# Performance work log

Hardware: AMD Instinct MI355X
Metric: run time of the kernel (lower is better)

The kernel has to match this reference:

```python
import jax, jax.numpy as jnp
import numpy as np

GROUPS = 32
EPS = 1e-5


def setup_inputs() -> dict:
    key = jax.random.key(0)
    ks = jax.random.split(key, 7)
    B, C, H, W = 32, 512, 32, 32
    x = jax.random.normal(ks[0], (B, C, H, W), dtype=jnp.float32)
    # GroupNorm affine params
    gn_w = jnp.ones((C,), dtype=jnp.float32)
    gn_b = jnp.zeros((C,), dtype=jnp.float32)
    # 1x1 Conv1d == matmul over channel dim
    qkv_w = jax.random.normal(ks[1], (3 * C, C), dtype=jnp.float32) * (C ** -0.5)
    qkv_b = jax.random.normal(ks[2], (3 * C,), dtype=jnp.float32) * 0.02
    proj_w = jax.random.normal(ks[3], (C, C), dtype=jnp.float32) * (C ** -0.5)
    proj_b = jax.random.normal(ks[4], (C,), dtype=jnp.float32) * 0.02
    return {"x": x, "gn_w": gn_w, "gn_b": gn_b, "qkv_w": qkv_w,
            "qkv_b": qkv_b, "proj_w": proj_w, "proj_b": proj_b}


def _group_norm(x, w, b):
    B, C, H, W = x.shape
    xg = x.reshape(B, GROUPS, C // GROUPS, H, W)
    mean = xg.mean(axis=(2, 3, 4), keepdims=True)
    var = xg.var(axis=(2, 3, 4), keepdims=True)
    xg = (xg - mean) * jax.lax.rsqrt(var + EPS)
    return xg.reshape(B, C, H, W) * w[None, :, None, None] + b[None, :, None, None]


def reference(x, gn_w, gn_b, qkv_w, qkv_b, proj_w, proj_b):
    B, C, H, W = x.shape
    h = _group_norm(x, gn_w, gn_b).reshape(B, C, H * W)  # [B, C, N]
    qkv = jnp.einsum('oc,bcn->bon', qkv_w, h) + qkv_b[None, :, None]  # [B, 3C, N]
    q, k, v = jnp.split(qkv, 3, axis=1)
    scale = C ** (-0.5)
    # scores: q^T k  -> [B, N, N]
    attn = jax.nn.softmax(jnp.einsum('bcn,bcm->bnm', q, k) * scale, axis=-1)
    # h = v @ attn^T -> [B, C, N]
    h = jnp.einsum('bcm,bnm->bcn', v, attn)
    h = jnp.einsum('oc,bcn->bon', proj_w, h) + proj_b[None, :, None]
    return x + h.reshape(B, C, H, W)
```

## Files before the change

### kernel.cpp

```cpp
#include <hip/hip_runtime.h>
#include <stdint.h>

typedef __bf16 bf16;
typedef __bf16 bf16x4 __attribute__((ext_vector_type(4)));
typedef __bf16 bf16x8 __attribute__((ext_vector_type(8)));
typedef float f32x4 __attribute__((ext_vector_type(4)));

#define CN 524288
#define NPIX 1024
#define CCH 512

__device__ __forceinline__ void gload_lds16(const void* g, void* l) {
  auto gp = reinterpret_cast<const __attribute__((address_space(1))) uint32_t*>(
      reinterpret_cast<uintptr_t>(g));
  auto lp = reinterpret_cast<__attribute__((address_space(3))) uint32_t*>(
      static_cast<uint32_t>(reinterpret_cast<uintptr_t>(l)));
  __builtin_amdgcn_global_load_lds(gp, lp, 16, 0, 0);
}

template<int EPI>
__global__ __launch_bounds__(512, 2)
void gemm_bt(const bf16* __restrict__ A, int lda, long long sA,
             const bf16* __restrict__ Bt, int ldb, long long sB,
             char* __restrict__ Cp, long long sC,
             char* __restrict__ C2p, long long sC2,
             const float* __restrict__ bias,
             const float* __restrict__ resid,
             int K, float scale)
{
  __shared__ __align__(16) bf16 As[2 * 16384];
  __shared__ __align__(16) bf16 Bs[2 * 16384];
  const int t = threadIdx.x;
  const int w = t >> 6;
  const int l = t & 63;
  const int z = blockIdx.z;
  A  += (long long)z * sA;
  Bt += (long long)z * sB;
  Cp += (long long)z * sC;
  if (C2p) C2p += (long long)z * sC2;
  const float* residb = (EPI == 3) ? (resid + (long long)z * CN) : nullptr;

  const int row0 = blockIdx.x * 256;
  const int col0 = blockIdx.y * 256;
  const int wr = w >> 2;
  const int wc = w & 3;

  f32x4 acc[8][4] = {};

  const int wv  = w;
  const int srow = (l >> 3);
  const int segp = ((l & 7) ^ srow) << 3;
  const bf16* baseA = A  + (long long)(row0 + wv * 8 + srow) * lda + segp;
  const bf16* baseB = Bt + (long long)(col0 + wv * 8 + srow) * ldb + segp;

  auto stageA = [&](int kt1, int buf, int c) {
    gload_lds16(baseA + (long long)c * 64 * lda + kt1 * 64,
                &As[buf * 16384 + c * 4096 + wv * 512]);
  };
  auto stageB = [&](int kt1, int buf, int c) {
    gload_lds16(baseB + (long long)c * 64 * ldb + kt1 * 64,
                &Bs[buf * 16384 + c * 4096 + wv * 512]);
  };

  const int lrow = l & 15;
  const int lx = l & 7;
  const int s0 = (((l >> 4)) ^ lx) << 3;
  const int s1 = (((l >> 4) + 4) ^ lx) << 3;

  const int nt = K >> 6;

  #pragma unroll
  for (int c = 0; c < 4; ++c) stageB(0, 0, c);
  #pragma unroll
  for (int c = 0; c < 4; ++c) stageA(0, 0, c);

  #pragma unroll 1
  for (int kt = 0; kt < nt; ++kt) {
    const int cur = kt & 1, nxt = cur ^ 1;
    const bool pf = (kt + 1) < nt;
    if (pf) {
      #pragma unroll
      for (int c = 0; c < 4; ++c) stageB(kt + 1, nxt, c);
      asm volatile("s_waitcnt vmcnt(4)" ::: "memory");
    } else {
      asm volatile("s_waitcnt vmcnt(0)" ::: "memory");
    }
    __builtin_amdgcn_sched_barrier(0);
    __builtin_amdgcn_s_barrier();
    asm volatile("" ::: "memory");

    const int ca = cur * 16384;
    bf16x8 bF0[4], bF1[4], aF0[4], aF1[4];
    #pragma unroll
    for (int nf = 0; nf < 4; ++nf) {
      const int r = wc * 64 + nf * 16 + lrow;
      bF0[nf] = *(const bf16x8*)&Bs[ca + r * 64 + s0];
      bF1[nf] = *(const bf16x8*)&Bs[ca + r * 64 + s1];
    }
    #pragma unroll
    for (int mf = 0; mf < 4; ++mf) {
      const int r = wr * 128 + mf * 16 + lrow;
      aF0[mf] = *(const bf16x8*)&As[ca + r * 64 + s0];
      aF1[mf] = *(const bf16x8*)&As[ca + r * 64 + s1];
    }
    __builtin_amdgcn_s_setprio(1);
    #pragma unroll
    for (int mf = 0; mf < 4; ++mf)
      #pragma unroll
      for (int nf = 0; nf < 4; ++nf)
        acc[mf][nf] = __builtin_amdgcn_mfma_f32_16x16x32_bf16(
            aF1[mf], bF1[nf],
            __builtin_amdgcn_mfma_f32_16x16x32_bf16(aF0[mf], bF0[nf], acc[mf][nf], 0, 0, 0),
            0, 0, 0);
    __builtin_amdgcn_s_setprio(0);
    if (pf) {
      #pragma unroll
      for (int c = 0; c < 4; ++c) stageA(kt + 1, nxt, c);
    }
    #pragma unroll
    for (int mf = 0; mf < 4; ++mf) {
      const int r = wr * 128 + 64 + mf * 16 + lrow;
      aF0[mf] = *(const bf16x8*)&As[ca + r * 64 + s0];
      aF1[mf] = *(const bf16x8*)&As[ca + r * 64 + s1];
    }
    __builtin_amdgcn_s_setprio(1);
    #pragma unroll
    for (int mf = 0; mf < 4; ++mf)
      #pragma unroll
      for (int nf = 0; nf < 4; ++nf)
        acc[4 + mf][nf] = __builtin_amdgcn_mfma_f32_16x16x32_bf16(
            aF1[mf], bF1[nf],
            __builtin_amdgcn_mfma_f32_16x16x32_bf16(aF0[mf], bF0[nf], acc[4 + mf][nf], 0, 0, 0),
            0, 0, 0);
    __builtin_amdgcn_s_setprio(0);
    asm volatile("" ::: "memory");
    __builtin_amdgcn_sched_barrier(0);
    __builtin_amdgcn_s_barrier();
  }

  (void)scale;
  const int ci = (l >> 4) * 4;
  const int cj = l & 15;
  #pragma unroll
  for (int mf = 0; mf < 8; ++mf) {
    const int i0 = row0 + wr * 128 + mf * 16 + ci;
    #pragma unroll
    for (int nf = 0; nf < 4; ++nf) {
      const int j = col0 + wc * 64 + nf * 16 + cj;
      const f32x4 a = acc[mf][nf];
      if constexpr (EPI == 0) {
        const float bj = bias[j];
        if (j < NPIX) {
          bf16* q = (bf16*)Cp;
          #pragma unroll
          for (int r = 0; r < 4; ++r)
            q[(i0 + r) * NPIX + j] = (bf16)(a[r] + bj);
        } else {
          bf16* vb = (bf16*)C2p;
          #pragma unroll
          for (int r = 0; r < 4; ++r)
            vb[(j - NPIX) * NPIX + (i0 + r)] = (bf16)(a[r] + bj);
        }
      } else if constexpr (EPI == 1) {
        bf16* sp = (bf16*)Cp;
        #pragma unroll
        for (int r = 0; r < 4; ++r)
          sp[(i0 + r) * NPIX + j] = (bf16)(a[r] * scale);
      } else if constexpr (EPI == 2) {
        bf16* hp = (bf16*)Cp;
        #pragma unroll
        for (int r = 0; r < 4; ++r)
          hp[(i0 + r) * CCH + j] = (bf16)a[r];
      } else {
        float* op = (float*)Cp;
        #pragma unroll
        for (int r = 0; r < 4; ++r)
          op[(i0 + r) * NPIX + j] = a[r] + bias[i0 + r] + residb[(i0 + r) * NPIX + j];
      }
    }
  }
}

__global__ __launch_bounds__(256)
void gn_fused(const float* __restrict__ x, const float* __restrict__ gw,
              const float* __restrict__ gb, bf16* __restrict__ hnT)
{
  __shared__ float xs[16 * 1024];
  __shared__ float red[8];
  const int b = blockIdx.x >> 5;
  const int g = blockIdx.x & 31;
  const float* xp = x + ((long long)b * CCH + g * 16) * NPIX;
  const int t = threadIdx.x;

  float4* xsv = (float4*)xs;
  const float4* gv = (const float4*)xp;
  float s = 0.f, ss = 0.f;
  #pragma unroll
  for (int i = 0; i < 16; ++i) {
    float4 v = gv[t + i * 256];
    xsv[t + i * 256] = v;
    s  += v.x + v.y + v.z + v.w;
    ss += v.x * v.x + v.y * v.y + v.z * v.z + v.w * v.w;
  }
  #pragma unroll
  for (int o = 32; o; o >>= 1) { s += __shfl_xor(s, o); ss += __shfl_xor(ss, o); }
  if ((t & 63) == 0) { red[t >> 6] = s; red[4 + (t >> 6)] = ss; }
  __syncthreads();
  s  = red[0] + red[1] + red[2] + red[3];
  ss = red[4] + red[5] + red[6] + red[7];
  const float mean = s * (1.f / 16384.f);
  const float var  = ss * (1.f / 16384.f) - mean * mean;
  const float rstd = rsqrtf(var + 1e-5f);

  float ac[16], bc[16];
  #pragma unroll
  for (int c = 0; c < 16; ++c) {
    const float wv = gw[g * 16 + c] * rstd;
    ac[c] = wv;
    bc[c] = gb[g * 16 + c] - mean * wv;
  }

  bf16* hp = hnT + (long long)b * CN + g * 16;
  #pragma unroll
  for (int r = 0; r < 4; ++r) {
    const int n = t + r * 256;
    bf16x8 o0, o1;
    #pragma unroll
    for (int c = 0; c < 8; ++c)
      o0[c] = (bf16)(xs[c * 1024 + n] * ac[c] + bc[c]);
    #pragma unroll
    for (int c = 0; c < 8; ++c)
      o1[c] = (bf16)(xs[(8 + c) * 1024 + n] * ac[8 + c] + bc[8 + c]);
    *(bf16x8*)&hp[(long long)n * CCH]     = o0;
    *(bf16x8*)&hp[(long long)n * CCH + 8] = o1;
  }
}

__global__ __launch_bounds__(256)
void softmax_rows(bf16* __restrict__ scores)
{
  bf16* p = scores + (long long)blockIdx.x * NPIX;
  const int t = threadIdx.x;
  const bf16x4 v = *(const bf16x4*)(p + t * 4);
  float f0 = (float)v[0], f1 = (float)v[1], f2 = (float)v[2], f3 = (float)v[3];
  float m = fmaxf(fmaxf(f0, f1), fmaxf(f2, f3));
  #pragma unroll
  for (int o = 32; o; o >>= 1) m = fmaxf(m, __shfl_xor(m, o));
  __shared__ float red[4];
  if ((t & 63) == 0) red[t >> 6] = m;
  __syncthreads();
  m = fmaxf(fmaxf(red[0], red[1]), fmaxf(red[2], red[3]));
  const float e0 = __expf(f0 - m), e1 = __expf(f1 - m);
  const float e2 = __expf(f2 - m), e3 = __expf(f3 - m);
  float s = e0 + e1 + e2 + e3;
  #pragma unroll
  for (int o = 32; o; o >>= 1) s += __shfl_xor(s, o);
  __syncthreads();
  if ((t & 63) == 0) red[t >> 6] = s;
  __syncthreads();
  s = red[0] + red[1] + red[2] + red[3];
  const float inv = 1.f / s;
  bf16x4 ov;
  ov[0] = (bf16)(e0 * inv); ov[1] = (bf16)(e1 * inv);
  ov[2] = (bf16)(e2 * inv); ov[3] = (bf16)(e3 * inv);
  *(bf16x4*)(p + t * 4) = ov;
}

__global__ __launch_bounds__(256)
void cvt_weights(const float* __restrict__ qw, const float* __restrict__ pw,
                 bf16* __restrict__ qwb, bf16* __restrict__ pwb)
{
  const int i = blockIdx.x * 256 + threadIdx.x;
  if (i < 3 * CCH * CCH) qwb[i] = (bf16)qw[i];
  if (i < CCH * CCH) pwb[i] = (bf16)pw[i];
}

extern "C" void kernel_launch(void* const* d_in, const int* in_sizes, int n_in,
                              void* d_out, int out_size, void* d_ws, size_t ws_size,
                              hipStream_t stream)
{
  const float* x      = (const float*)d_in[0];
  const float* gn_w   = (const float*)d_in[1];
  const float* gn_b   = (const float*)d_in[2];
  const float* qkv_w  = (const float*)d_in[3];
  const float* qkv_b  = (const float*)d_in[4];
  const float* proj_w = (const float*)d_in[5];
  const float* proj_b = (const float*)d_in[6];
  float* out = (float*)d_out;
  (void)in_sizes; (void)n_in; (void)out_size;

  char* ws = (char*)d_ws;
  size_t off = 0;
  auto alloc = [&](size_t bytes) -> char* {
    char* p = ws + off;
    off += (bytes + 255) & ~(size_t)255;
    return p;
  };
  bf16* qkv_wb  = (bf16*)alloc(3 * 512 * 512 * 2);
  bf16* proj_wb = (bf16*)alloc(512 * 512 * 2);
  const size_t fixed = off;
  const size_t per = 1048576ull + 2097152ull + 1048576ull + 2097152ull + 1048576ull;
  int Bc = 32;
  if (ws_size > fixed) {
    size_t fit = (ws_size - fixed) / per;
    if (fit < 32) Bc = (int)fit;
  } else {
    Bc = 0;
  }
  if (Bc < 1) Bc = 1;

  bf16*  hnT    = (bf16*) alloc((size_t)Bc * 1048576);
  bf16*  qkT    = (bf16*) alloc((size_t)Bc * 2097152);
  bf16*  vbuf   = (bf16*) alloc((size_t)Bc * 1048576);
  bf16*  scores = (bf16*) alloc((size_t)Bc * 2097152);
  bf16*  hvT    = (bf16*) alloc((size_t)Bc * 1048576);

  cvt_weights<<<dim3(3072), 256, 0, stream>>>(qkv_w, proj_w, qkv_wb, proj_wb);

  const float scale = 0.044194173824159216f;
  for (int b0 = 0; b0 < 32; b0 += Bc) {
    const int bc = (32 - b0 < Bc) ? (32 - b0) : Bc;
    const float* xb = x + (size_t)b0 * CN;

    gn_fused<<<dim3(bc * 32), 256, 0, stream>>>(xb, gn_w, gn_b, hnT);

    gemm_bt<0><<<dim3(4, 6, bc), 512, 0, stream>>>(
        hnT, 512, 524288, qkv_wb, 512, 0,
        (char*)qkT, 2097152, (char*)vbuf, 1048576, qkv_b, nullptr, 512, 1.f);

    gemm_bt<1><<<dim3(4, 4, bc), 512, 0, stream>>>(
        qkT, 1024, 1048576, qkT + 512, 1024, 1048576,
        (char*)scores, 2097152, nullptr, 0, nullptr, nullptr, 512, scale);

    softmax_rows<<<dim3(bc * 1024), 256, 0, stream>>>(scores);

    gemm_bt<2><<<dim3(4, 2, bc), 512, 0, stream>>>(
        scores, 1024, 1048576, vbuf, 1024, 524288,
        (char*)hvT, 1048576, nullptr, 0, nullptr, nullptr, 1024, 1.f);

    gemm_bt<3><<<dim3(2, 4, bc), 512, 0, stream>>>(
        proj_wb, 512, 0, hvT, 512, 524288,
        (char*)(out + (size_t)b0 * CN), 2097152, nullptr, 0, proj_b, xb, 512, 1.f);
  }
}
```

Before: 266.6 us.

## Fuse softmax into QK^T and PV GEMM epilogues, drop separate softmax kernel

The QK^T GEMM epilogue now writes exp(score*scale) as bf16 and produces per-tile partial row sums through LDS into a small stats buffer. The PV GEMM epilogue divides each output row by the summed partials. This removes the standalone softmax kernel and its full read and write of the score matrix. It skips the row-max subtraction, so it relies on scores staying small enough not to overflow exp. It also rounds the numerator to bf16 before the sum is taken.

```diff
diff --git a/kernel.cpp b/kernel.cpp
--- a/kernel.cpp
+++ b/kernel.cpp
@@ -26,6 +26,7 @@
              char* __restrict__ C2p, long long sC2,
              const float* __restrict__ bias,
              const float* __restrict__ resid,
+             float* __restrict__ pst,
              int K, float scale)
 {
   __shared__ __align__(16) bf16 As[2 * 16384];
@@ -138,44 +139,79 @@
     __builtin_amdgcn_s_barrier();
   }
 
-  (void)scale;
   const int ci = (l >> 4) * 4;
   const int cj = l & 15;
+
+  if constexpr (EPI == 1) {
+    bf16* sp = (bf16*)Cp;
+    float* part = (float*)As;
+    #pragma unroll
+    for (int mf = 0; mf < 8; ++mf) {
+      const int lr0 = wr * 128 + mf * 16 + ci;
+      #pragma unroll
+      for (int r = 0; r < 4; ++r) {
+        float s = 0.f;
+        #pragma unroll
+        for (int nf = 0; nf < 4; ++nf) {
+          const int j = col0 + wc * 64 + nf * 16 + cj;
+          const float u = __expf(acc[mf][nf][r] * scale);
+          const bf16 ub = (bf16)u;
+          sp[(row0 + lr0 + r) * NPIX + j] = ub;
+          s += (float)ub;
+        }
+        s += __shfl_xor(s, 1); s += __shfl_xor(s, 2);
+        s += __shfl_xor(s, 4); s += __shfl_xor(s, 8);
+        if (cj == 0) part[wc * 256 + lr0 + r] = s;
+      }
+    }
+    __syncthreads();
+    if (t < 256)
+      pst[((long long)z * 4 + blockIdx.y) * 1024 + row0 + t]
+          = part[t] + part[256 + t] + part[512 + t] + part[768 + t];
+    return;
+  }
+
   #pragma unroll
   for (int mf = 0; mf < 8; ++mf) {
     const int i0 = row0 + wr * 128 + mf * 16 + ci;
-    #pragma unroll
-    for (int nf = 0; nf < 4; ++nf) {
-      const int j = col0 + wc * 64 + nf * 16 + cj;
-      const f32x4 a = acc[mf][nf];
-      if constexpr (EPI == 0) {
-        const float bj = bias[j];
-        if (j < NPIX) {
-          bf16* q = (bf16*)Cp;
+    if constexpr (EPI == 2) {
+      const float* pz = pst + (long long)z * 4096;
+      #pragma unroll
+      for (int r = 0; r < 4; ++r) {
+        const int row = i0 + r;
+        const float is = 1.f / (pz[row] + pz[1024 + row] +
+                                pz[2048 + row] + pz[3072 + row]);
+        bf16* hp = (bf16*)Cp;
+        #pragma unroll
+        for (int nf = 0; nf < 4; ++nf) {
+          const int j = col0 + wc * 64 + nf * 16 + cj;
+          hp[row * CCH + j] = (bf16)(acc[mf][nf][r] * is);
+        }
+      }
+    } else {
+      #pragma unroll
+      for (int nf = 0; nf < 4; ++nf) {
+        const int j = col0 + wc * 64 + nf * 16 + cj;
+        const f32x4 a = acc[mf][nf];
+        if constexpr (EPI == 0) {
+          const float bj = bias[j];
+          if (j < NPIX) {
+            bf16* q = (bf16*)Cp;
+            #pragma unroll
+            for (int r = 0; r < 4; ++r)
+              q[(i0 + r) * NPIX + j] = (bf16)(a[r] + bj);
+          } else {
+            bf16* vb = (bf16*)C2p;
+            #pragma unroll
+            for (int r = 0; r < 4; ++r)
+              vb[(j - NPIX) * NPIX + (i0 + r)] = (bf16)(a[r] + bj);
+          }
+        } else {
+          float* op = (float*)Cp;
           #pragma unroll
           for (int r = 0; r < 4; ++r)
-            q[(i0 + r) * NPIX + j] = (bf16)(a[r] + bj);
-        } else {
-          bf16* vb = (bf16*)C2p;
-          #pragma unroll
-          for (int r = 0; r < 4; ++r)
-            vb[(j - NPIX) * NPIX + (i0 + r)] = (bf16)(a[r] + bj);
+            op[(i0 + r) * NPIX + j] = a[r] + bias[i0 + r] + residb[(i0 + r) * NPIX + j];
         }
-      } else if constexpr (EPI == 1) {
-        bf16* sp = (bf16*)Cp;
-        #pragma unroll
-        for (int r = 0; r < 4; ++r)
-          sp[(i0 + r) * NPIX + j] = (bf16)(a[r] * scale);
-      } else if constexpr (EPI == 2) {
-        bf16* hp = (bf16*)Cp;
-        #pragma unroll
-        for (int r = 0; r < 4; ++r)
-          hp[(i0 + r) * CCH + j] = (bf16)a[r];
-      } else {
-        float* op = (float*)Cp;
-        #pragma unroll
-        for (int r = 0; r < 4; ++r)
-          op[(i0 + r) * NPIX + j] = a[r] + bias[i0 + r] + residb[(i0 + r) * NPIX + j];
       }
     }
   }
@@ -234,36 +270,6 @@
     *(bf16x8*)&hp[(long long)n * CCH]     = o0;
     *(bf16x8*)&hp[(long long)n * CCH + 8] = o1;
   }
-}
-
-__global__ __launch_bounds__(256)
-void softmax_rows(bf16* __restrict__ scores)
-{
-  bf16* p = scores + (long long)blockIdx.x * NPIX;
-  const int t = threadIdx.x;
-  const bf16x4 v = *(const bf16x4*)(p + t * 4);
-  float f0 = (float)v[0], f1 = (float)v[1], f2 = (float)v[2], f3 = (float)v[3];
-  float m = fmaxf(fmaxf(f0, f1), fmaxf(f2, f3));
-  #pragma unroll
-  for (int o = 32; o; o >>= 1) m = fmaxf(m, __shfl_xor(m, o));
-  __shared__ float red[4];
-  if ((t & 63) == 0) red[t >> 6] = m;
-  __syncthreads();
-  m = fmaxf(fmaxf(red[0], red[1]), fmaxf(red[2], red[3]));
-  const float e0 = __expf(f0 - m), e1 = __expf(f1 - m);
-  const float e2 = __expf(f2 - m), e3 = __expf(f3 - m);
-  float s = e0 + e1 + e2 + e3;
-  #pragma unroll
-  for (int o = 32; o; o >>= 1) s += __shfl_xor(s, o);
-  __syncthreads();
-  if ((t & 63) == 0) red[t >> 6] = s;
-  __syncthreads();
-  s = red[0] + red[1] + red[2] + red[3];
-  const float inv = 1.f / s;
-  bf16x4 ov;
-  ov[0] = (bf16)(e0 * inv); ov[1] = (bf16)(e1 * inv);
-  ov[2] = (bf16)(e2 * inv); ov[3] = (bf16)(e3 * inv);
-  *(bf16x4*)(p + t * 4) = ov;
 }
 
 __global__ __launch_bounds__(256)
@@ -299,7 +305,8 @@
   bf16* qkv_wb  = (bf16*)alloc(3 * 512 * 512 * 2);
   bf16* proj_wb = (bf16*)alloc(512 * 512 * 2);
   const size_t fixed = off;
-  const size_t per = 1048576ull + 2097152ull + 1048576ull + 2097152ull + 1048576ull;
+  const size_t per = 1048576ull + 2097152ull + 1048576ull + 2097152ull
+                   + 1048576ull + 16384ull;
   int Bc = 32;
   if (ws_size > fixed) {
     size_t fit = (ws_size - fixed) / per;
@@ -312,8 +319,9 @@
   bf16*  hnT    = (bf16*) alloc((size_t)Bc * 1048576);
   bf16*  qkT    = (bf16*) alloc((size_t)Bc * 2097152);
   bf16*  vbuf   = (bf16*) alloc((size_t)Bc * 1048576);
-  bf16*  scores = (bf16*) alloc((size_t)Bc * 2097152);
+  bf16*  ubuf   = (bf16*) alloc((size_t)Bc * 2097152);
   bf16*  hvT    = (bf16*) alloc((size_t)Bc * 1048576);
+  float* pstats = (float*)alloc((size_t)Bc * 16384);
 
   cvt_weights<<<dim3(3072), 256, 0, stream>>>(qkv_w, proj_w, qkv_wb, proj_wb);
 
@@ -326,20 +334,22 @@
 
     gemm_bt<0><<<dim3(4, 6, bc), 512, 0, stream>>>(
         hnT, 512, 524288, qkv_wb, 512, 0,
-        (char*)qkT, 2097152, (char*)vbuf, 1048576, qkv_b, nullptr, 512, 1.f);
+        (char*)qkT, 2097152, (char*)vbuf, 1048576, qkv_b, nullptr, nullptr,
+        512, 1.f);
 
     gemm_bt<1><<<dim3(4, 4, bc), 512, 0, stream>>>(
         qkT, 1024, 1048576, qkT + 512, 1024, 1048576,
-        (char*)scores, 2097152, nullptr, 0, nullptr, nullptr, 512, scale);
-
-    softmax_rows<<<dim3(bc * 1024), 256, 0, stream>>>(scores);
+        (char*)ubuf, 2097152, nullptr, 0, nullptr, nullptr, pstats,
+        512, scale);
 
     gemm_bt<2><<<dim3(4, 2, bc), 512, 0, stream>>>(
-        scores, 1024, 1048576, vbuf, 1024, 524288,
-        (char*)hvT, 1048576, nullptr, 0, nullptr, nullptr, 1024, 1.f);
+        ubuf, 1024, 1048576, vbuf, 1024, 524288,
+        (char*)hvT, 1048576, nullptr, 0, nullptr, nullptr, pstats,
+        1024, 1.f);
 
     gemm_bt<3><<<dim3(2, 4, bc), 512, 0, stream>>>(
         proj_wb, 512, 0, hvT, 512, 524288,
-        (char*)(out + (size_t)b0 * CN), 2097152, nullptr, 0, proj_b, xb, 512, 1.f);
-  }
-}
+        (char*)(out + (size_t)b0 * CN), 2097152, nullptr, 0, proj_b, xb,
+        nullptr, 512, 1.f);
+  }
+}
```

Result: faster. 245.1 us (-8.1%).
